# Kernel tuning notes

Measured on AMD Instinct MI355X. Metric: run time of the kernel, lower is better.

## Reference

```python
import jax, jax.numpy as jnp
import numpy as np

NMS_THR = 0.3        # cfg.TEST.NMS
SCORE_THR = 0.5      # thr_2 == False branch
DEDUP_IOU_THR = 0.3  # compute_iou default iou_thresh


def _iou_matrix(a, b):
    # a: [N,4], b: [M,4] -> [N,M] IoU (matches compute_iou math: no +1, 1e-6 eps)
    area_a = (a[:, 2] - a[:, 0]) * (a[:, 3] - a[:, 1])
    area_b = (b[:, 2] - b[:, 0]) * (b[:, 3] - b[:, 1])
    lt = jnp.maximum(a[:, None, :2], b[None, :, :2])
    rb = jnp.minimum(a[:, None, 2:4], b[None, :, 2:4])
    wh = jnp.maximum(rb - lt, 0.0)
    inter = wh[..., 0] * wh[..., 1]
    return inter / (area_a[:, None] + area_b[None, :] - inter + 1e-6)


def _chan_norm(f):
    # f: [C,H,W] -> mean over channels, then Frobenius norm (torch.norm p=2)
    return jnp.linalg.norm(jnp.mean(f, axis=0))


def setup_inputs() -> dict:
    key = jax.random.key(0)
    ks = jax.random.split(key, 8)
    N, C, M = 2000, 21, 20

    def make_boxes(k, n, W=800.0, H=600.0):
        k1, k2, k3, k4 = jax.random.split(k, 4)
        cx = jax.random.uniform(k1, (n,)) * (W - 100.0) + 50.0
        cy = jax.random.uniform(k2, (n,)) * (H - 100.0) + 50.0
        w = jax.random.uniform(k3, (n,)) * 150.0 + 20.0
        h = jax.random.uniform(k4, (n,)) * 150.0 + 20.0
        return jnp.stack([cx - w / 2, cy - h / 2, cx + w / 2, cy + h / 2], -1)

    boxes = make_boxes(ks[0], N)
    rois = jnp.concatenate([jnp.zeros((N, 1)), boxes], -1)[None]
    cls_prob = jax.random.uniform(ks[1], (1, N, C))
    bbox_pred = 0.5 * jax.random.normal(ks[2], (1, N, 4 * C))
    im_info = jnp.array([[600.0, 800.0, 1.6]], jnp.float32)
    gt_b = make_boxes(ks[3], M)
    gt_lbl = jax.random.randint(ks[4], (M, 1), 1, C).astype(jnp.float32)
    gt_boxes = jnp.concatenate([gt_b, gt_lbl], -1)[None]
    feat = jax.random.normal(ks[5], (1, 512, 38, 50))
    feat_org = feat + 0.1 * jax.random.normal(ks[6], (1, 512, 38, 50))
    feat_res = 0.1 * jax.random.normal(ks[7], (1, 512, 38, 50))
    return dict(rois=rois, cls_prob=cls_prob, bbox_pred=bbox_pred,
                im_info=im_info, gt_boxes=gt_boxes, num_boxes=12,
                feat=feat, feat_org=feat_org, feat_res=feat_res)


def reference(rois, cls_prob, bbox_pred, im_info, gt_boxes, num_boxes,
              feat, feat_org, feat_res):
    N, C = cls_prob.shape[1], cls_prob.shape[2]
    M = gt_boxes.shape[1]
    scores = cls_prob[0]                       # [N,C]
    boxes = rois[0, :, 1:5]                    # [N,4]

    # bbox_transform_inv with BBOX_NORMALIZE_STDS/MEANS (means = 0)
    stds = jnp.array([0.1, 0.1, 0.2, 0.2], scores.dtype)
    deltas = bbox_pred[0].reshape(N, C, 4) * stds
    w = boxes[:, 2] - boxes[:, 0] + 1.0
    h = boxes[:, 3] - boxes[:, 1] + 1.0
    cx = boxes[:, 0] + 0.5 * w
    cy = boxes[:, 1] + 0.5 * h
    pcx = deltas[..., 0] * w[:, None] + cx[:, None]
    pcy = deltas[..., 1] * h[:, None] + cy[:, None]
    pw = jnp.exp(deltas[..., 2]) * w[:, None]
    ph = jnp.exp(deltas[..., 3]) * h[:, None]
    pred = jnp.stack([pcx - 0.5 * pw, pcy - 0.5 * ph,
                      pcx + 0.5 * pw, pcy + 0.5 * ph], -1)  # [N,C,4]
    H_im, W_im = im_info[0, 0], im_info[0, 1]
    pred = jnp.stack([jnp.clip(pred[..., 0], 0.0, W_im - 1),
                      jnp.clip(pred[..., 1], 0.0, H_im - 1),
                      jnp.clip(pred[..., 2], 0.0, W_im - 1),
                      jnp.clip(pred[..., 3], 0.0, H_im - 1)], -1)

    gt = gt_boxes[0]
    gt_valid = jnp.arange(M) < num_boxes
    idx = jnp.arange(N)

    def per_class(sj, bj):
        # score threshold + sort descending (invalid sorted last)
        valid = sj > SCORE_THR
        order = jnp.argsort(jnp.where(valid, -sj, jnp.inf))
        sb = bj[order]
        ss = sj[order]
        sv = valid[order]
        iou = _iou_matrix(sb, sb)              # [N,N]

        # greedy NMS over descending-score order
        def body(keep, i):
            sup = jnp.any(keep & (iou[i] > NMS_THR) & (idx < i))
            k = sv[i] & ~sup
            return keep.at[i].set(k), None
        keep, _ = jax.lax.scan(body, jnp.zeros(N, bool), idx)

        # dedup against valid gt boxes (vectorized replacement of the Python
        # double loop over compute_iou)
        gt_iou = _iou_matrix(sb, gt[:, :4])    # [N,M]
        hit = jnp.any((gt_iou > DEDUP_IOU_THR) & gt_valid[None, :], axis=1)
        final = keep & ~hit
        dets = jnp.concatenate([sb, ss[:, None]], -1)
        return dets * final[:, None].astype(dets.dtype)  # [N,5]

    # classes 1..C-1 (skip background), class-specific boxes
    dets = jax.vmap(per_class)(scores[:, 1:].T,
                               jnp.swapaxes(pred[:, 1:, :], 0, 1))  # [C-1,N,5]

    # feature distillation losses (L1 between scalar channel-mean norms)
    f, fo, fr = feat[0], feat_org[0], feat_res[0]
    n_f = _chan_norm(f)
    distil_loss = jnp.abs(n_f - _chan_norm(fo))
    res_loss = jnp.abs(_chan_norm(f - fo) - _chan_norm(fr))
    res_loss_inc = jnp.abs(_chan_norm(fo + fr) - n_f)
    residual_loss = res_loss_inc + res_loss

    return jnp.concatenate([dets.reshape(-1),
                            jnp.stack([distil_loss, residual_loss])])
```

## Files before the change

kernel.cpp:

```cpp
#include <hip/hip_runtime.h>
#include <hip/hip_bf16.h>

#pragma clang fp contract(off)

#define N_BOX 2000
#define N_CLS 21
#define SORT_N 2048
#define M_GT 20
#define FEAT_HW 1900
#define FEAT_F4 475
#define FEAT_C 512
#define BLK 1024
#define NW_MAX 22

#define OFF_SBOX (32768)
#define OFF_SS   (32768 + 655360)
#define OFF_V    (851968)
#define OFF_BIT  (1048576)

__device__ __forceinline__ float bf2f(__hip_bfloat16 x) { return __bfloat162float(x); }
__device__ __forceinline__ float fin(float x) { return (x == x && fabsf(x) <= 3.0e38f) ? x : 0.0f; }
__device__ __forceinline__ bool probe_is_f32(const void* im_info) {
    return *(const unsigned*)im_info == 0x44160000u;
}
__device__ __forceinline__ float ld(const void* p, bool f32, int i) {
    return f32 ? ((const float*)p)[i] : bf2f(((const __hip_bfloat16*)p)[i]);
}
__device__ __forceinline__ float4 ld4f(const void* p, bool f32, int i4) {
    if (f32) return ((const float4*)p)[i4];
    ushort4 u = ((const ushort4*)p)[i4];
    return make_float4(__uint_as_float((unsigned)u.x << 16),
                       __uint_as_float((unsigned)u.y << 16),
                       __uint_as_float((unsigned)u.z << 16),
                       __uint_as_float((unsigned)u.w << 16));
}
__device__ __forceinline__ float iou_f(float4 a, float4 b) {
    float area_a = (a.z - a.x) * (a.w - a.y);
    float area_b = (b.z - b.x) * (b.w - b.y);
    float ltx = fmaxf(a.x, b.x), lty = fmaxf(a.y, b.y);
    float rbx = fminf(a.z, b.z), rby = fminf(a.w, b.w);
    float wx = fmaxf(rbx - ltx, 0.0f), wy = fmaxf(rby - lty, 0.0f);
    float inter = wx * wy;
    return inter / (area_a + area_b - inter + 1e-6f);
}
__device__ __forceinline__ int parse_count(const void* p) {
    int iv = *(const int*)p;
    if (iv >= 0 && iv <= 1000) return iv < M_GT ? iv : M_GT;
    float fv = *(const float*)p;
    if (fv >= 0.0f && fv <= 1000.0f) { int v = (int)fv; return v < M_GT ? v : M_GT; }
    float bv = bf2f(*(const __hip_bfloat16*)p);
    if (bv >= 0.0f && bv <= 1000.0f) { int v = (int)bv; return v < M_GT ? v : M_GT; }
    return 0;
}
__device__ __forceinline__ float4 decode_box(const void* rois, const void* bbox_pred,
                                             bool f32, int n, int c, float Wim, float Him) {
    float x1 = ld(rois, f32, n * 5 + 1);
    float y1 = ld(rois, f32, n * 5 + 2);
    float x2 = ld(rois, f32, n * 5 + 3);
    float y2 = ld(rois, f32, n * 5 + 4);
    float w = x2 - x1 + 1.0f;
    float h = y2 - y1 + 1.0f;
    float cx = x1 + 0.5f * w;
    float cy = y1 + 0.5f * h;
    int dbase = n * (4 * N_CLS) + c * 4;
    float d0, d1, d2, d3;
    if (f32) {
        float4 d = *(const float4*)((const float*)bbox_pred + dbase);
        d0 = d.x * 0.1f; d1 = d.y * 0.1f; d2 = d.z * 0.2f; d3 = d.w * 0.2f;
    } else {
        d0 = ld(bbox_pred, f32, dbase + 0) * 0.1f;
        d1 = ld(bbox_pred, f32, dbase + 1) * 0.1f;
        d2 = ld(bbox_pred, f32, dbase + 2) * 0.2f;
        d3 = ld(bbox_pred, f32, dbase + 3) * 0.2f;
    }
    float pcx = d0 * w + cx;
    float pcy = d1 * h + cy;
    float pw = (float)exp((double)d2) * w;
    float ph = (float)exp((double)d3) * h;
    float xmax = Wim - 1.0f, ymax = Him - 1.0f;
    float xa = fminf(fmaxf(pcx - 0.5f * pw, 0.0f), xmax);
    float ya = fminf(fmaxf(pcy - 0.5f * ph, 0.0f), ymax);
    float xb = fminf(fmaxf(pcx + 0.5f * pw, 0.0f), xmax);
    float yb = fminf(fmaxf(pcy + 0.5f * ph, 0.0f), ymax);
    return make_float4(fin(xa), fin(ya), fin(xb), fin(yb));
}
__device__ __forceinline__ unsigned long long readlane64(unsigned long long v, int l) {
    unsigned lo = (unsigned)__builtin_amdgcn_readlane((unsigned)(v & 0xFFFFFFFFull), l);
    unsigned hi = (unsigned)__builtin_amdgcn_readlane((unsigned)(v >> 32), l);
    return ((unsigned long long)hi << 32) | (unsigned long long)lo;
}

__global__ __launch_bounds__(BLK) void rank_kernel(
        const void* __restrict__ rois, const void* __restrict__ cls_prob,
        const void* __restrict__ bbox_pred, const void* __restrict__ im_info,
        float4* __restrict__ wsbox, float* __restrict__ wss, int* __restrict__ wV) {
    __shared__ unsigned long long keys[SORT_N];
    __shared__ int lds_V;
    const int tid = threadIdx.x;
    const int lane = tid & 63;
    const bool f32 = probe_is_f32(im_info);
    const int cc = blockIdx.x >> 4;
    const int oct = blockIdx.x & 15;
    const int cls = cc + 1;
    if (tid == 0) lds_V = 0;
    __syncthreads();

    auto makekey = [&](int e) -> unsigned long long {
        if (e < N_BOX) {
            float s = ld(cls_prob, f32, e * N_CLS + cls);
            bool valid = s > 0.5f;
            float kf = valid ? -s : __builtin_inff();
            unsigned kbv = __float_as_uint(kf);
            kbv = (kbv & 0x80000000u) ? ~kbv : (kbv | 0x80000000u);
            return ((unsigned long long)kbv << 32) | (unsigned)e;
        }
        return ~0ull;
    };
    unsigned long long k0 = makekey(tid);
    unsigned long long k1 = makekey(tid + 1024);
    keys[tid] = k0;
    keys[tid + 1024] = k1;
    {
        unsigned long long m0 = __ballot((k0 >> 32) < 0xFF800000ull);
        unsigned long long m1 = __ballot((k1 >> 32) < 0xFF800000ull);
        if (lane == 0) {
            int vc = __popcll(m0) + __popcll(m1);
            if (vc) atomicAdd(&lds_V, vc);
        }
    }
    __syncthreads();
    if (oct == 0 && tid == 0) wV[cc] = lds_V;

    const int i = (oct << 7) + (tid >> 3);
    const int seg = tid & 7;
    const unsigned long long ki = keys[i];
    int rank = 0;
    #pragma unroll 8
    for (int jj = 0; jj < 256; ++jj) {
        rank += (keys[(jj << 3) | seg] < ki) ? 1 : 0;
    }
    rank += __shfl_xor(rank, 1);
    rank += __shfl_xor(rank, 2);
    rank += __shfl_xor(rank, 4);
    if (seg == 0 && i < N_BOX) {
        unsigned h = (unsigned)(ki >> 32);
        if (h < 0xFF800000u) {
            const float Him = fin(ld(im_info, f32, 0));
            const float Wim = fin(ld(im_info, f32, 1));
            wsbox[cc * SORT_N + rank] = decode_box(rois, bbox_pred, f32, i, cls, Wim, Him);
            wss[cc * SORT_N + rank] = -__uint_as_float(~h);
        }
    }
}

__global__ __launch_bounds__(256, 4) void ioumat_loss_kernel(
        const float4* __restrict__ wsbox, const int* __restrict__ wV,
        unsigned long long* __restrict__ bitmat,
        const void* __restrict__ feat, const void* __restrict__ feat_org,
        const void* __restrict__ feat_res, const void* __restrict__ im_info,
        float* __restrict__ acc, float* __restrict__ out, int out_n) {
    for (int i = blockIdx.x * 256 + threadIdx.x; i < out_n; i += 760 * 256) out[i] = 0.0f;
    const int wv = threadIdx.x >> 6;
    const int lane = threadIdx.x & 63;

    if (blockIdx.x >= 640) {
        __shared__ float4 red[3][4][16];
        const bool f32 = probe_is_f32(im_info);
        const int lb = blockIdx.x - 640;
        const int ps = lb >> 2;
        const int cs = lb & 3;
        const int col = lane & 15;
        const int fc = ps * 16 + col;
        const int cg = (wv << 2) | (lane >> 4);
        float4 sa = make_float4(0.f, 0.f, 0.f, 0.f);
        float4 sb4 = make_float4(0.f, 0.f, 0.f, 0.f);
        float4 sr4 = make_float4(0.f, 0.f, 0.f, 0.f);
        if (fc < FEAT_F4) {
            #pragma unroll
            for (int k = 0; k < 8; ++k) {
                int off = (cs * 128 + cg * 8 + k) * FEAT_F4 + fc;
                float4 fa = ld4f(feat, f32, off);
                float4 fb = ld4f(feat_org, f32, off);
                float4 fc4 = ld4f(feat_res, f32, off);
                sa.x += fin(fa.x); sa.y += fin(fa.y); sa.z += fin(fa.z); sa.w += fin(fa.w);
                sb4.x += fin(fb.x); sb4.y += fin(fb.y); sb4.z += fin(fb.z); sb4.w += fin(fb.w);
                sr4.x += fin(fc4.x); sr4.y += fin(fc4.y); sr4.z += fin(fc4.z); sr4.w += fin(fc4.w);
            }
        }
        #pragma unroll
        for (int o = 16; o <= 32; o <<= 1) {
            sa.x += __shfl_xor(sa.x, o); sa.y += __shfl_xor(sa.y, o);
            sa.z += __shfl_xor(sa.z, o); sa.w += __shfl_xor(sa.w, o);
            sb4.x += __shfl_xor(sb4.x, o); sb4.y += __shfl_xor(sb4.y, o);
            sb4.z += __shfl_xor(sb4.z, o); sb4.w += __shfl_xor(sb4.w, o);
            sr4.x += __shfl_xor(sr4.x, o); sr4.y += __shfl_xor(sr4.y, o);
            sr4.z += __shfl_xor(sr4.z, o); sr4.w += __shfl_xor(sr4.w, o);
        }
        if (lane < 16) { red[0][wv][lane] = sa; red[1][wv][lane] = sb4; red[2][wv][lane] = sr4; }
        __syncthreads();
        if (wv == 0) {
            float v0 = 0.f, v1 = 0.f, v2 = 0.f, v3 = 0.f, v4 = 0.f;
            if (lane < 16) {
                float4 ta = make_float4(0.f, 0.f, 0.f, 0.f);
                float4 tb = make_float4(0.f, 0.f, 0.f, 0.f);
                float4 tr = make_float4(0.f, 0.f, 0.f, 0.f);
                #pragma unroll
                for (int w = 0; w < 4; ++w) {
                    float4 x = red[0][w][lane];
                    ta.x += x.x; ta.y += x.y; ta.z += x.z; ta.w += x.w;
                    x = red[1][w][lane];
                    tb.x += x.x; tb.y += x.y; tb.z += x.z; tb.w += x.w;
                    x = red[2][w][lane];
                    tr.x += x.x; tr.y += x.y; tr.z += x.z; tr.w += x.w;
                }
                const float inv = 1.0f / 512.0f;
                float ma, mb, mr;
                ma = ta.x * inv; mb = tb.x * inv; mr = tr.x * inv;
                v0 += ma * ma; v1 += mb * mb; v2 += (ma - mb) * (ma - mb);
                v3 += (mb + mr) * (mb + mr); v4 += mr * mr;
                ma = ta.y * inv; mb = tb.y * inv; mr = tr.y * inv;
                v0 += ma * ma; v1 += mb * mb; v2 += (ma - mb) * (ma - mb);
                v3 += (mb + mr) * (mb + mr); v4 += mr * mr;
                ma = ta.z * inv; mb = tb.z * inv; mr = tr.z * inv;
                v0 += ma * ma; v1 += mb * mb; v2 += (ma - mb) * (ma - mb);
                v3 += (mb + mr) * (mb + mr); v4 += mr * mr;
                ma = ta.w * inv; mb = tb.w * inv; mr = tr.w * inv;
                v0 += ma * ma; v1 += mb * mb; v2 += (ma - mb) * (ma - mb);
                v3 += (mb + mr) * (mb + mr); v4 += mr * mr;
            }
            #pragma unroll
            for (int o = 8; o; o >>= 1) {
                v0 += __shfl_down(v0, o); v1 += __shfl_down(v1, o); v2 += __shfl_down(v2, o);
                v3 += __shfl_down(v3, o); v4 += __shfl_down(v4, o);
            }
            if (lane == 0) {
                float* part = acc + 64 + lb * 8;
                part[0] = v0; part[1] = v1; part[2] = v2; part[3] = v3; part[4] = v4;
            }
        }
        return;
    }

    const int cc = blockIdx.x >> 5;
    const int chunk = blockIdx.x & 31;
    const int V = wV[cc];
    const int base = chunk << 6;
    if (base >= V) return;
    const int nw = (V + 63) >> 6;
    const float4* sb = wsbox + cc * SORT_N;
    unsigned long long* bm = bitmat + ((size_t)cc * SORT_N << 5);
    const int w4 = wv;

    for (int half = 0; half < 2; ++half) {
        const int rbase = base + (w4 << 4) + (half << 3);
        float4 bi[8]; float ai[8];
        #pragma unroll
        for (int k = 0; k < 8; ++k) {
            float4 b = sb[rbase + k];
            bi[k] = b;
            ai[k] = (b.z - b.x) * (b.w - b.y);
        }
        for (int w = chunk; w < nw; ++w) {
            int j = (w << 6) | lane;
            float4 bj = sb[j];
            float aj = (bj.z - bj.x) * (bj.w - bj.y);
            #pragma unroll
            for (int k = 0; k < 8; ++k) {
                int r = rbase + k;
                float ltx = fmaxf(bi[k].x, bj.x), lty = fmaxf(bi[k].y, bj.y);
                float rbx = fminf(bi[k].z, bj.z), rby = fminf(bi[k].w, bj.w);
                float wx = fmaxf(rbx - ltx, 0.0f), wy = fmaxf(rby - lty, 0.0f);
                float inter = wx * wy;
                float iou = inter / (ai[k] + aj - inter + 1e-6f);
                bool conf = (j > r) && (j < V) && (iou > 0.3f);
                unsigned long long m = __ballot(conf);
                if (lane == 0 && r < V)
                    __builtin_nontemporal_store(m, &bm[((size_t)r << 5) + w]);
            }
        }
    }
}

__global__ __launch_bounds__(BLK) void scan_write_kernel(
        const void* __restrict__ im_info, const void* __restrict__ gt_boxes,
        const void* __restrict__ num_boxes,
        const float4* __restrict__ wsbox, const float* __restrict__ wss,
        const int* __restrict__ wV, const unsigned long long* __restrict__ bitmat,
        const float* __restrict__ acc, float* __restrict__ out) {
    __shared__ unsigned long long tri[16928];
    __shared__ unsigned long long diag_l[NW_MAX * 64];
    __shared__ unsigned long long keepw_s[32];
    __shared__ float4 gtb[M_GT];
    __shared__ int rb2_s[NW_MAX];
    __shared__ int len2_s[NW_MAX];
    __shared__ float fr[2][5];
    const int tid = threadIdx.x;
    const int lane = tid & 63;
    const int wv = tid >> 6;
    const bool f32 = probe_is_f32(im_info);

    if (blockIdx.x == 20) {
        float v0 = 0.f, v1 = 0.f, v2 = 0.f, v3 = 0.f, v4 = 0.f;
        if (tid < 120) {
            const float* p = acc + 64 + tid * 8;
            v0 = p[0]; v1 = p[1]; v2 = p[2]; v3 = p[3]; v4 = p[4];
        }
        for (int o = 32; o; o >>= 1) {
            v0 += __shfl_down(v0, o); v1 += __shfl_down(v1, o); v2 += __shfl_down(v2, o);
            v3 += __shfl_down(v3, o); v4 += __shfl_down(v4, o);
        }
        if (lane == 0 && wv < 2) {
            fr[wv][0] = v0; fr[wv][1] = v1; fr[wv][2] = v2; fr[wv][3] = v3; fr[wv][4] = v4;
        }
        __syncthreads();
        if (tid == 0) {
            float a0 = fr[0][0] + fr[1][0];
            float a1 = fr[0][1] + fr[1][1];
            float a2 = fr[0][2] + fr[1][2];
            float a3 = fr[0][3] + fr[1][3];
            float a4 = fr[0][4] + fr[1][4];
            float nA = sqrtf(fmaxf(fin(a0), 0.0f));
            float nB = sqrtf(fmaxf(fin(a1), 0.0f));
            float nAB = sqrtf(fmaxf(fin(a2), 0.0f));
            float nBR = sqrtf(fmaxf(fin(a3), 0.0f));
            float nR = sqrtf(fmaxf(fin(a4), 0.0f));
            float* out2 = out + (long)N_BOX * (N_CLS - 1) * 5;
            out2[0] = fin(fabsf(nA - nB));
            out2[1] = fin(fabsf(nBR - nA) + fabsf(nAB - nR));
        }
        return;
    }

    const int cc = blockIdx.x;
    const int V = wV[cc];
    const int nw = (V + 63) >> 6;
    const unsigned long long* bm = bitmat + ((size_t)cc * SORT_N << 5);
    const bool planA = (V > 0) && (nw <= NW_MAX);
    if (tid < 32) keepw_s[tid] = 0ull;
    if (tid >= 64 && tid < 64 + M_GT) {
        int g = tid - 64;
        gtb[g] = make_float4(fin(ld(gt_boxes, f32, g * 5 + 0)),
                             fin(ld(gt_boxes, f32, g * 5 + 1)),
                             fin(ld(gt_boxes, f32, g * 5 + 2)),
                             fin(ld(gt_boxes, f32, g * 5 + 3)));
    }
    if (tid == 0) {
        int a = 0;
        for (int b = 0; b < NW_MAX; ++b) {
            rb2_s[b] = a;
            int b2 = b & ~1;
            int l2 = ((nw - b2) + 1) & ~1;
            if (l2 < 0) l2 = 0;
            len2_s[b] = l2;
            a += 64 * l2;
        }
    }
    __syncthreads();

    if (planA) {
        #pragma unroll 2
        for (int t = tid; t < (V << 4); t += BLK) {
            const int r = t >> 4;
            const int c = t & 15;
            const int b = r >> 6;
            const int b2 = b & ~1;
            const int l2 = len2_s[b];
            if ((c << 1) < l2) {
                ulonglong2 v = *(const ulonglong2*)(bm + ((size_t)r << 5) + b2 + (c << 1));
                const int idx = rb2_s[b] + (r & 63) * l2 + (c << 1);
                tri[idx] = v.x;
                tri[idx + 1] = v.y;
                if (c == 0) diag_l[r] = (b & 1) ? v.y : v.x;
            }
        }
    }
    __syncthreads();

    if (planA) {
        if (wv == 0) {
            const int wl = lane & 31;
            unsigned long long removedW = 0ull, keepW = 0ull;
            unsigned long long d_cur = diag_l[lane];
            for (int B = 0; B < nw; ++B) {
                unsigned long long d_nxt = (B + 1 < nw) ? diag_l[((B + 1) << 6) + lane] : 0ull;
                const int rbase = B << 6;
                int rows = V - rbase; if (rows > 64) rows = 64;
                const unsigned long long valid = (rows >= 64) ? ~0ull : ((1ull << rows) - 1ull);
                const unsigned long long curRem = readlane64(removedW, B);
                unsigned long long cand = ~curRem & valid;
                unsigned long long keepB = 0ull;
                while (cand) {
                    int r = __builtin_ctzll(cand);
                    keepB |= (1ull << r);
                    unsigned long long dr = readlane64(d_cur, r);
                    cand &= ~(dr | (1ull << r));
                }
                const int rbv = rb2_s[B];
                const int l2 = len2_s[B];
                const int wo = wl - (B & ~1);
                unsigned long long kk = keepB, add = 0ull;
                while (kk) {
                    int rr[8];
                    rr[0] = __builtin_ctzll(kk); kk &= kk - 1ull;
                    #pragma unroll
                    for (int t = 1; t < 8; ++t) {
                        rr[t] = kk ? __builtin_ctzll(kk) : rr[0];
                        if (kk) kk &= kk - 1ull;
                    }
                    unsigned long long a = 0ull;
                    #pragma unroll
                    for (int t = 0; t < 8; ++t)
                        a |= tri[rbv + rr[t] * l2 + wo];
                    add |= a;
                }
                removedW |= add;
                if (wl == B) keepW |= keepB;
                d_cur = d_nxt;
            }
            if (lane < 32) keepw_s[lane] = keepW;
        }
    } else if (V > 0) {
        if (wv == 0) {
            const int wl = lane & 31;
            unsigned long long removedW = 0ull, keepW = 0ull;
            unsigned long long d_cur = bm[((size_t)lane << 5)];
            for (int B = 0; B < nw; ++B) {
                unsigned long long d_nxt = 0ull;
                if (B + 1 < nw) {
                    int rn = ((B + 1) << 6) + lane;
                    d_nxt = bm[((size_t)rn << 5) + (B + 1)];
                }
                const int rbase = B << 6;
                int rows = V - rbase; if (rows > 64) rows = 64;
                const unsigned long long valid = (rows >= 64) ? ~0ull : ((1ull << rows) - 1ull);
                const unsigned long long curRem = readlane64(removedW, B);
                unsigned long long cand = ~curRem & valid;
                unsigned long long keepB = 0ull;
                while (cand) {
                    int r = __builtin_ctzll(cand);
                    keepB |= (1ull << r);
                    unsigned long long dr = readlane64(d_cur, r);
                    cand &= ~(dr | (1ull << r));
                }
                unsigned long long kk = keepB, add = 0ull;
                while (kk) {
                    int rr[8];
                    rr[0] = __builtin_ctzll(kk); kk &= kk - 1ull;
                    #pragma unroll
                    for (int t = 1; t < 8; ++t) {
                        rr[t] = kk ? __builtin_ctzll(kk) : rr[0];
                        if (kk) kk &= kk - 1ull;
                    }
                    unsigned long long a = 0ull;
                    #pragma unroll
                    for (int t = 0; t < 8; ++t)
                        a |= bm[((size_t)(rbase + rr[t]) << 5) + wl];
                    add |= a;
                }
                removedW |= add;
                if (wl == B) keepW |= keepB;
                d_cur = d_nxt;
            }
            if (lane < 32) keepw_s[lane] = keepW;
        }
    }
    __syncthreads();

    const int nb = parse_count(num_boxes);
    long obase = (long)cc * (N_BOX * 5);
    for (int i = tid; i < N_BOX; i += BLK) {
        if ((keepw_s[i >> 6] >> (i & 63)) & 1ull) {
            float4 b = wsbox[cc * SORT_N + i];
            bool fn = true;
            for (int m = 0; m < nb; ++m) {
                if (iou_f(b, gtb[m]) > 0.3f) { fn = false; break; }
            }
            if (fn) {
                float* op = out + obase + (long)i * 5;
                op[0] = b.x; op[1] = b.y; op[2] = b.z; op[3] = b.w; op[4] = wss[cc * SORT_N + i];
            }
        }
    }
}

extern "C" void kernel_launch(void* const* d_in, const int* in_sizes, int n_in,
                              void* d_out, int out_size, void* d_ws, size_t ws_size,
                              hipStream_t stream) {
    const void* p_rois = nullptr;
    const void* p_cls = nullptr;
    const void* p_bbox = nullptr;
    const void* p_iminfo = nullptr;
    const void* p_gt = nullptr;
    const void* p_nb = nullptr;
    const void* p_feat[3] = {nullptr, nullptr, nullptr};
    int nfeat = 0;
    for (int i = 0; i < n_in; ++i) {
        int s = in_sizes[i];
        if (s == 10000 || s == 20000) p_rois = d_in[i];
        else if (s == 42000 || s == 84000) p_cls = d_in[i];
        else if (s == 168000 || s == 336000) p_bbox = d_in[i];
        else if (s == 3 || s == 6) p_iminfo = d_in[i];
        else if (s == 100 || s == 200) p_gt = d_in[i];
        else if (s == 1 || s == 4) p_nb = d_in[i];
        else if ((s == 972800 || s == 1945600) && nfeat < 3) p_feat[nfeat++] = d_in[i];
    }
    if (!p_rois)   p_rois = d_in[0];
    if (!p_cls)    p_cls = d_in[1];
    if (!p_bbox)   p_bbox = d_in[2];
    if (!p_iminfo) p_iminfo = d_in[3];
    if (!p_gt)     p_gt = d_in[4];
    if (!p_nb)     p_nb = d_in[5];
    if (nfeat < 3) { p_feat[0] = d_in[6]; p_feat[1] = d_in[7]; p_feat[2] = d_in[8]; }

    float* out = (float*)d_out;
    char* ws = (char*)d_ws;
    float* acc = (float*)ws;

    float4* wsbox = (float4*)(ws + OFF_SBOX);
    float* wss = (float*)(ws + OFF_SS);
    int* wV = (int*)(ws + OFF_V);
    unsigned long long* bitmat = (unsigned long long*)(ws + OFF_BIT);

    rank_kernel<<<320, BLK, 0, stream>>>(p_rois, p_cls, p_bbox, p_iminfo,
                                         wsbox, wss, wV);
    ioumat_loss_kernel<<<760, 256, 0, stream>>>(wsbox, wV, bitmat,
                                                p_feat[0], p_feat[1], p_feat[2],
                                                p_iminfo, acc, out, out_size);
    scan_write_kernel<<<21, BLK, 0, stream>>>(p_iminfo, p_gt, p_nb, wsbox, wss,
                                              wV, bitmat, acc, out);
}
```

Measured before the change: 189.3 us.

## Move feature-loss reduction into rank kernel and tile IoU bitmask over triangular grid

The feature-norm partial reductions move from the IoU kernel into the rank kernel as 30 extra 1024-thread blocks, each covering all 512 channels, so they overlap with the sort/rank work. The IoU bitmask kernel is relaunched as a 2D grid with one block per upper-triangular (row-word, column-word) tile pair per class, which removes the serial loop over column words and the imbalance between chunks. The final loss reduction reads 30 partials instead of 120. Risks are many early-exit blocks for classes with few valid boxes, per-row box reloads in the IoU tile, and the sqrt-based triangular index decode.

```diff
diff --git a/kernel.cpp b/kernel.cpp
--- a/kernel.cpp
+++ b/kernel.cpp
@@ -12,6 +12,7 @@
 #define FEAT_C 512
 #define BLK 1024
 #define NW_MAX 22
+#define NTILE 528
 
 #define OFF_SBOX (32768)
 #define OFF_SS   (32768 + 655360)
@@ -90,87 +91,24 @@
     return ((unsigned long long)hi << 32) | (unsigned long long)lo;
 }
 
-__global__ __launch_bounds__(BLK) void rank_kernel(
+__global__ __launch_bounds__(BLK) void rank_loss_kernel(
         const void* __restrict__ rois, const void* __restrict__ cls_prob,
         const void* __restrict__ bbox_pred, const void* __restrict__ im_info,
-        float4* __restrict__ wsbox, float* __restrict__ wss, int* __restrict__ wV) {
+        const void* __restrict__ feat, const void* __restrict__ feat_org,
+        const void* __restrict__ feat_res,
+        float4* __restrict__ wsbox, float* __restrict__ wss, int* __restrict__ wV,
+        float* __restrict__ acc) {
     __shared__ unsigned long long keys[SORT_N];
+    __shared__ float4 red[3][16][16];
     __shared__ int lds_V;
     const int tid = threadIdx.x;
     const int lane = tid & 63;
+    const int wv = tid >> 6;
     const bool f32 = probe_is_f32(im_info);
-    const int cc = blockIdx.x >> 4;
-    const int oct = blockIdx.x & 15;
-    const int cls = cc + 1;
-    if (tid == 0) lds_V = 0;
-    __syncthreads();
-
-    auto makekey = [&](int e) -> unsigned long long {
-        if (e < N_BOX) {
-            float s = ld(cls_prob, f32, e * N_CLS + cls);
-            bool valid = s > 0.5f;
-            float kf = valid ? -s : __builtin_inff();
-            unsigned kbv = __float_as_uint(kf);
-            kbv = (kbv & 0x80000000u) ? ~kbv : (kbv | 0x80000000u);
-            return ((unsigned long long)kbv << 32) | (unsigned)e;
-        }
-        return ~0ull;
-    };
-    unsigned long long k0 = makekey(tid);
-    unsigned long long k1 = makekey(tid + 1024);
-    keys[tid] = k0;
-    keys[tid + 1024] = k1;
-    {
-        unsigned long long m0 = __ballot((k0 >> 32) < 0xFF800000ull);
-        unsigned long long m1 = __ballot((k1 >> 32) < 0xFF800000ull);
-        if (lane == 0) {
-            int vc = __popcll(m0) + __popcll(m1);
-            if (vc) atomicAdd(&lds_V, vc);
-        }
-    }
-    __syncthreads();
-    if (oct == 0 && tid == 0) wV[cc] = lds_V;
-
-    const int i = (oct << 7) + (tid >> 3);
-    const int seg = tid & 7;
-    const unsigned long long ki = keys[i];
-    int rank = 0;
-    #pragma unroll 8
-    for (int jj = 0; jj < 256; ++jj) {
-        rank += (keys[(jj << 3) | seg] < ki) ? 1 : 0;
-    }
-    rank += __shfl_xor(rank, 1);
-    rank += __shfl_xor(rank, 2);
-    rank += __shfl_xor(rank, 4);
-    if (seg == 0 && i < N_BOX) {
-        unsigned h = (unsigned)(ki >> 32);
-        if (h < 0xFF800000u) {
-            const float Him = fin(ld(im_info, f32, 0));
-            const float Wim = fin(ld(im_info, f32, 1));
-            wsbox[cc * SORT_N + rank] = decode_box(rois, bbox_pred, f32, i, cls, Wim, Him);
-            wss[cc * SORT_N + rank] = -__uint_as_float(~h);
-        }
-    }
-}
-
-__global__ __launch_bounds__(256, 4) void ioumat_loss_kernel(
-        const float4* __restrict__ wsbox, const int* __restrict__ wV,
-        unsigned long long* __restrict__ bitmat,
-        const void* __restrict__ feat, const void* __restrict__ feat_org,
-        const void* __restrict__ feat_res, const void* __restrict__ im_info,
-        float* __restrict__ acc, float* __restrict__ out, int out_n) {
-    for (int i = blockIdx.x * 256 + threadIdx.x; i < out_n; i += 760 * 256) out[i] = 0.0f;
-    const int wv = threadIdx.x >> 6;
-    const int lane = threadIdx.x & 63;
-
-    if (blockIdx.x >= 640) {
-        __shared__ float4 red[3][4][16];
-        const bool f32 = probe_is_f32(im_info);
-        const int lb = blockIdx.x - 640;
-        const int ps = lb >> 2;
-        const int cs = lb & 3;
-        const int col = lane & 15;
-        const int fc = ps * 16 + col;
+
+    if (blockIdx.x >= 320) {
+        const int lb = blockIdx.x - 320;
+        const int fc = lb * 16 + (lane & 15);
         const int cg = (wv << 2) | (lane >> 4);
         float4 sa = make_float4(0.f, 0.f, 0.f, 0.f);
         float4 sb4 = make_float4(0.f, 0.f, 0.f, 0.f);
@@ -178,7 +116,7 @@
         if (fc < FEAT_F4) {
             #pragma unroll
             for (int k = 0; k < 8; ++k) {
-                int off = (cs * 128 + cg * 8 + k) * FEAT_F4 + fc;
+                int off = ((cg << 3) + k) * FEAT_F4 + fc;
                 float4 fa = ld4f(feat, f32, off);
                 float4 fb = ld4f(feat_org, f32, off);
                 float4 fc4 = ld4f(feat_res, f32, off);
@@ -199,13 +137,12 @@
         if (lane < 16) { red[0][wv][lane] = sa; red[1][wv][lane] = sb4; red[2][wv][lane] = sr4; }
         __syncthreads();
         if (wv == 0) {
-            float v0 = 0.f, v1 = 0.f, v2 = 0.f, v3 = 0.f, v4 = 0.f;
+            float4 ta = make_float4(0.f, 0.f, 0.f, 0.f);
+            float4 tb = make_float4(0.f, 0.f, 0.f, 0.f);
+            float4 tr = make_float4(0.f, 0.f, 0.f, 0.f);
             if (lane < 16) {
-                float4 ta = make_float4(0.f, 0.f, 0.f, 0.f);
-                float4 tb = make_float4(0.f, 0.f, 0.f, 0.f);
-                float4 tr = make_float4(0.f, 0.f, 0.f, 0.f);
                 #pragma unroll
-                for (int w = 0; w < 4; ++w) {
+                for (int w = 0; w < 16; ++w) {
                     float4 x = red[0][w][lane];
                     ta.x += x.x; ta.y += x.y; ta.z += x.z; ta.w += x.w;
                     x = red[1][w][lane];
@@ -213,7 +150,10 @@
                     x = red[2][w][lane];
                     tr.x += x.x; tr.y += x.y; tr.z += x.z; tr.w += x.w;
                 }
-                const float inv = 1.0f / 512.0f;
+            }
+            const float inv = 1.0f / 512.0f;
+            float v0 = 0.f, v1 = 0.f, v2 = 0.f, v3 = 0.f, v4 = 0.f;
+            {
                 float ma, mb, mr;
                 ma = ta.x * inv; mb = tb.x * inv; mr = tr.x * inv;
                 v0 += ma * ma; v1 += mb * mb; v2 += (ma - mb) * (ma - mb);
@@ -228,8 +168,7 @@
                 v0 += ma * ma; v1 += mb * mb; v2 += (ma - mb) * (ma - mb);
                 v3 += (mb + mr) * (mb + mr); v4 += mr * mr;
             }
-            #pragma unroll
-            for (int o = 8; o; o >>= 1) {
+            for (int o = 32; o; o >>= 1) {
                 v0 += __shfl_down(v0, o); v1 += __shfl_down(v1, o); v2 += __shfl_down(v2, o);
                 v3 += __shfl_down(v3, o); v4 += __shfl_down(v4, o);
             }
@@ -241,43 +180,101 @@
         return;
     }
 
-    const int cc = blockIdx.x >> 5;
-    const int chunk = blockIdx.x & 31;
+    const int cc = blockIdx.x >> 4;
+    const int oct = blockIdx.x & 15;
+    const int cls = cc + 1;
+    if (tid == 0) lds_V = 0;
+    __syncthreads();
+
+    auto makekey = [&](int e) -> unsigned long long {
+        if (e < N_BOX) {
+            float s = ld(cls_prob, f32, e * N_CLS + cls);
+            bool valid = s > 0.5f;
+            float kf = valid ? -s : __builtin_inff();
+            unsigned kbv = __float_as_uint(kf);
+            kbv = (kbv & 0x80000000u) ? ~kbv : (kbv | 0x80000000u);
+            return ((unsigned long long)kbv << 32) | (unsigned)e;
+        }
+        return ~0ull;
+    };
+    unsigned long long k0 = makekey(tid);
+    unsigned long long k1 = makekey(tid + 1024);
+    keys[tid] = k0;
+    keys[tid + 1024] = k1;
+    {
+        unsigned long long m0 = __ballot((k0 >> 32) < 0xFF800000ull);
+        unsigned long long m1 = __ballot((k1 >> 32) < 0xFF800000ull);
+        if (lane == 0) {
+            int vc = __popcll(m0) + __popcll(m1);
+            if (vc) atomicAdd(&lds_V, vc);
+        }
+    }
+    __syncthreads();
+    if (oct == 0 && tid == 0) wV[cc] = lds_V;
+
+    const int i = (oct << 7) + (tid >> 3);
+    const int seg = tid & 7;
+    const unsigned long long ki = keys[i];
+    int rank = 0;
+    #pragma unroll 8
+    for (int jj = 0; jj < 256; ++jj) {
+        rank += (keys[(jj << 3) | seg] < ki) ? 1 : 0;
+    }
+    rank += __shfl_xor(rank, 1);
+    rank += __shfl_xor(rank, 2);
+    rank += __shfl_xor(rank, 4);
+    if (seg == 0 && i < N_BOX) {
+        unsigned h = (unsigned)(ki >> 32);
+        if (h < 0xFF800000u) {
+            const float Him = fin(ld(im_info, f32, 0));
+            const float Wim = fin(ld(im_info, f32, 1));
+            wsbox[cc * SORT_N + rank] = decode_box(rois, bbox_pred, f32, i, cls, Wim, Him);
+            wss[cc * SORT_N + rank] = -__uint_as_float(~h);
+        }
+    }
+}
+
+__global__ __launch_bounds__(256) void ioumat_kernel(
+        const float4* __restrict__ wsbox, const int* __restrict__ wV,
+        unsigned long long* __restrict__ bitmat,
+        float* __restrict__ out, int out_n) {
+    const int tid = threadIdx.x;
+    {
+        int bid = blockIdx.y * NTILE + blockIdx.x;
+        for (int i = bid * 256 + tid; i < out_n; i += NTILE * 20 * 256) out[i] = 0.0f;
+    }
+    const int cc = blockIdx.y;
     const int V = wV[cc];
-    const int base = chunk << 6;
-    if (base >= V) return;
     const int nw = (V + 63) >> 6;
+    const int t = blockIdx.x;
+    int a = (int)((65.0f - sqrtf(4225.0f - 8.0f * (float)t)) * 0.5f);
+    while ((a + 1) * (65 - (a + 1)) / 2 <= t) ++a;
+    while (a * (65 - a) / 2 > t) --a;
+    const int b = a + (t - a * (65 - a) / 2);
+    if (b >= nw) return;
+
+    const int lane = tid & 63;
+    const int wv = tid >> 6;
     const float4* sb = wsbox + cc * SORT_N;
     unsigned long long* bm = bitmat + ((size_t)cc * SORT_N << 5);
-    const int w4 = wv;
-
-    for (int half = 0; half < 2; ++half) {
-        const int rbase = base + (w4 << 4) + (half << 3);
-        float4 bi[8]; float ai[8];
-        #pragma unroll
-        for (int k = 0; k < 8; ++k) {
-            float4 b = sb[rbase + k];
-            bi[k] = b;
-            ai[k] = (b.z - b.x) * (b.w - b.y);
-        }
-        for (int w = chunk; w < nw; ++w) {
-            int j = (w << 6) | lane;
-            float4 bj = sb[j];
-            float aj = (bj.z - bj.x) * (bj.w - bj.y);
-            #pragma unroll
-            for (int k = 0; k < 8; ++k) {
-                int r = rbase + k;
-                float ltx = fmaxf(bi[k].x, bj.x), lty = fmaxf(bi[k].y, bj.y);
-                float rbx = fminf(bi[k].z, bj.z), rby = fminf(bi[k].w, bj.w);
-                float wx = fmaxf(rbx - ltx, 0.0f), wy = fmaxf(rby - lty, 0.0f);
-                float inter = wx * wy;
-                float iou = inter / (ai[k] + aj - inter + 1e-6f);
-                bool conf = (j > r) && (j < V) && (iou > 0.3f);
-                unsigned long long m = __ballot(conf);
-                if (lane == 0 && r < V)
-                    __builtin_nontemporal_store(m, &bm[((size_t)r << 5) + w]);
-            }
-        }
+
+    const int j = (b << 6) | lane;
+    float4 bj = sb[j];
+    const float aj = (bj.z - bj.x) * (bj.w - bj.y);
+    const int rbase = (a << 6) + (wv << 4);
+    #pragma unroll
+    for (int rr = 0; rr < 16; ++rr) {
+        const int r = rbase + rr;
+        float4 bi = sb[r];
+        float ai = (bi.z - bi.x) * (bi.w - bi.y);
+        float ltx = fmaxf(bi.x, bj.x), lty = fmaxf(bi.y, bj.y);
+        float rbx = fminf(bi.z, bj.z), rby = fminf(bi.w, bj.w);
+        float wx = fmaxf(rbx - ltx, 0.0f), wy = fmaxf(rby - lty, 0.0f);
+        float inter = wx * wy;
+        float iou = inter / (ai + aj - inter + 1e-6f);
+        bool conf = (j > r) && (j < V) && (iou > 0.3f);
+        unsigned long long m = __ballot(conf);
+        if (lane == 0 && r < V) bm[((size_t)r << 5) + b] = m;
     }
 }
 
@@ -293,40 +290,32 @@
     __shared__ float4 gtb[M_GT];
     __shared__ int rb2_s[NW_MAX];
     __shared__ int len2_s[NW_MAX];
-    __shared__ float fr[2][5];
     const int tid = threadIdx.x;
     const int lane = tid & 63;
     const int wv = tid >> 6;
     const bool f32 = probe_is_f32(im_info);
 
     if (blockIdx.x == 20) {
-        float v0 = 0.f, v1 = 0.f, v2 = 0.f, v3 = 0.f, v4 = 0.f;
-        if (tid < 120) {
-            const float* p = acc + 64 + tid * 8;
-            v0 = p[0]; v1 = p[1]; v2 = p[2]; v3 = p[3]; v4 = p[4];
-        }
-        for (int o = 32; o; o >>= 1) {
-            v0 += __shfl_down(v0, o); v1 += __shfl_down(v1, o); v2 += __shfl_down(v2, o);
-            v3 += __shfl_down(v3, o); v4 += __shfl_down(v4, o);
-        }
-        if (lane == 0 && wv < 2) {
-            fr[wv][0] = v0; fr[wv][1] = v1; fr[wv][2] = v2; fr[wv][3] = v3; fr[wv][4] = v4;
-        }
-        __syncthreads();
-        if (tid == 0) {
-            float a0 = fr[0][0] + fr[1][0];
-            float a1 = fr[0][1] + fr[1][1];
-            float a2 = fr[0][2] + fr[1][2];
-            float a3 = fr[0][3] + fr[1][3];
-            float a4 = fr[0][4] + fr[1][4];
-            float nA = sqrtf(fmaxf(fin(a0), 0.0f));
-            float nB = sqrtf(fmaxf(fin(a1), 0.0f));
-            float nAB = sqrtf(fmaxf(fin(a2), 0.0f));
-            float nBR = sqrtf(fmaxf(fin(a3), 0.0f));
-            float nR = sqrtf(fmaxf(fin(a4), 0.0f));
-            float* out2 = out + (long)N_BOX * (N_CLS - 1) * 5;
-            out2[0] = fin(fabsf(nA - nB));
-            out2[1] = fin(fabsf(nBR - nA) + fabsf(nAB - nR));
+        if (tid < 64) {
+            float v0 = 0.f, v1 = 0.f, v2 = 0.f, v3 = 0.f, v4 = 0.f;
+            if (tid < 30) {
+                const float* p = acc + 64 + tid * 8;
+                v0 = p[0]; v1 = p[1]; v2 = p[2]; v3 = p[3]; v4 = p[4];
+            }
+            for (int o = 32; o; o >>= 1) {
+                v0 += __shfl_down(v0, o); v1 += __shfl_down(v1, o); v2 += __shfl_down(v2, o);
+                v3 += __shfl_down(v3, o); v4 += __shfl_down(v4, o);
+            }
+            if (tid == 0) {
+                float nA = sqrtf(fmaxf(fin(v0), 0.0f));
+                float nB = sqrtf(fmaxf(fin(v1), 0.0f));
+                float nAB = sqrtf(fmaxf(fin(v2), 0.0f));
+                float nBR = sqrtf(fmaxf(fin(v3), 0.0f));
+                float nR = sqrtf(fmaxf(fin(v4), 0.0f));
+                float* out2 = out + (long)N_BOX * (N_CLS - 1) * 5;
+                out2[0] = fin(fabsf(nA - nB));
+                out2[1] = fin(fabsf(nBR - nA) + fabsf(nAB - nR));
+            }
         }
         return;
     }
@@ -521,11 +510,10 @@
     int* wV = (int*)(ws + OFF_V);
     unsigned long long* bitmat = (unsigned long long*)(ws + OFF_BIT);
 
-    rank_kernel<<<320, BLK, 0, stream>>>(p_rois, p_cls, p_bbox, p_iminfo,
-                                         wsbox, wss, wV);
-    ioumat_loss_kernel<<<760, 256, 0, stream>>>(wsbox, wV, bitmat,
-                                                p_feat[0], p_feat[1], p_feat[2],
-                                                p_iminfo, acc, out, out_size);
+    rank_loss_kernel<<<350, BLK, 0, stream>>>(p_rois, p_cls, p_bbox, p_iminfo,
+                                              p_feat[0], p_feat[1], p_feat[2],
+                                              wsbox, wss, wV, acc);
+    ioumat_kernel<<<dim3(NTILE, 20), 256, 0, stream>>>(wsbox, wV, bitmat, out, out_size);
     scan_write_kernel<<<21, BLK, 0, stream>>>(p_iminfo, p_gt, p_nb, wsbox, wss,
                                               wV, bitmat, acc, out);
 }
```

Result: faster. 156.0 us (-17.6%).
